# Kernel optimization log

Hardware: AMD Instinct MI355X
Metric: run time of the kernel (lower is better)

Reference implementation:

```python
import jax, jax.numpy as jnp
import numpy as np
import math

B, H, W, C = 8, 64, 64, 512
HEADS, DHEAD = 8, 64
LN_EPS = 1e-5


def layer_norm(x, g, b):
    mu = jnp.mean(x, axis=-1, keepdims=True)
    var = jnp.var(x, axis=-1, keepdims=True)
    return (x - mu) * jax.lax.rsqrt(var + LN_EPS) * g + b


def l2norm(x):
    n = jnp.sqrt(jnp.sum(x * x, axis=-1, keepdims=True))
    return x / jnp.maximum(n, 1e-12)


def dwconv3x3(x, w):
    # x: (B,C,H,W), w: (C,1,3,3) depthwise
    return jax.lax.conv_general_dilated(
        x, w, window_strides=(1, 1), padding='SAME',
        feature_group_count=x.shape[1],
        dimension_numbers=('NCHW', 'OIHW', 'NCHW'))


def setup_inputs() -> dict:
    key = jax.random.key(0)
    ks = jax.random.split(key, 16)
    s = 1.0 / math.sqrt(C)
    inp = {
        'x_in': jax.random.normal(ks[0], (B, H, W, C), jnp.float32),
        'illu_fea_trans': jax.random.normal(ks[1], (B, H, W, C), jnp.float32),
        'sem_fea_trans': jax.random.normal(ks[2], (B, H, W, C), jnp.float32),
        # SIF 1x1 convs as (C_in, C_out) matrices
        'Wk_sif': jax.random.normal(ks[3], (C, C), jnp.float32) * s,
        'Wq_sif': jax.random.normal(ks[4], (C, C), jnp.float32) * s,
        'Wv_sif': jax.random.normal(ks[5], (C, C), jnp.float32) * s,
        'ln_g': jnp.ones((C,), jnp.float32),
        'ln_b': jnp.zeros((C,), jnp.float32),
        # FG_MSA linears (in, out)
        'Wq': jax.random.normal(ks[6], (C, HEADS * DHEAD), jnp.float32) * s,
        'Wk': jax.random.normal(ks[7], (C, HEADS * DHEAD), jnp.float32) * s,
        'Wv': jax.random.normal(ks[8], (C, HEADS * DHEAD), jnp.float32) * s,
        'rescale': jnp.ones((HEADS, 1, 1), jnp.float32),
        'proj_w': jax.random.normal(ks[9], (HEADS * DHEAD, C), jnp.float32) * s,
        'proj_b': jnp.zeros((C,), jnp.float32),
        # depthwise conv pos-emb
        'dw1': jax.random.normal(ks[10], (C, 1, 3, 3), jnp.float32) * (1.0 / 3.0),
        'dw2': jax.random.normal(ks[11], (C, 1, 3, 3), jnp.float32) * (1.0 / 3.0),
    }
    return inp


def sif(illu, sem, Wk_sif, Wq_sif, Wv_sif, ln_g, ln_b):
    # illu, sem: (B, N, C); channel (C x C) cross-attention
    Kn = layer_norm(illu @ Wk_sif, ln_g, ln_b)          # (B,N,C)
    Qn = layer_norm(sem @ Wq_sif, ln_g, ln_b)           # (B,N,C)
    V = illu @ Wv_sif                                    # (B,N,C)
    Ab = jnp.einsum('bni,bnj->bij', Qn, Kn) / math.sqrt(C)  # (B,C,C)
    Ab = jax.nn.softmax(Ab, axis=-1)
    # (Ab @ V^T)^T + V ; SIF_FFN treated as identity (source not provided)
    return jnp.einsum('bij,bnj->bni', Ab, V) + V


def reference(x_in, illu_fea_trans, sem_fea_trans, Wk_sif, Wq_sif, Wv_sif,
              ln_g, ln_b, Wq, Wk, Wv, rescale, proj_w, proj_b, dw1, dw2):
    b, h, w, c = x_in.shape
    n = h * w
    x = x_in.reshape(b, n, c)
    q_inp = x @ Wq
    k_inp = x @ Wk
    v_inp = x @ Wv

    prior = sif(illu_fea_trans.reshape(b, n, c), sem_fea_trans.reshape(b, n, c),
                Wk_sif, Wq_sif, Wv_sif, ln_g, ln_b)      # (B,N,C)

    def split_heads(t):  # (b,n,h*d) -> (b,h,n,d)
        return t.reshape(b, n, HEADS, DHEAD).transpose(0, 2, 1, 3)

    q, k, v, g = map(split_heads, (q_inp, k_inp, v_inp, prior))
    v = v * g
    # transpose to (b,h,d,n), L2-normalize over n
    q = l2norm(q.transpose(0, 1, 3, 2))
    k = l2norm(k.transpose(0, 1, 3, 2))
    v = v.transpose(0, 1, 3, 2)
    attn = jnp.einsum('bhdn,bhen->bhde', k, q) * rescale  # (b,h,d,d)
    attn = jax.nn.softmax(attn, axis=-1)
    o = jnp.einsum('bhde,bhen->bhdn', attn, v)            # (b,h,d,n)
    o = o.transpose(0, 3, 1, 2).reshape(b, n, HEADS * DHEAD)
    out_c = (o @ proj_w + proj_b).reshape(b, h, w, c)

    vmap = v_inp.reshape(b, h, w, c).transpose(0, 3, 1, 2)  # NCHW
    p = dwconv3x3(vmap, dw1)
    p = jax.nn.gelu(p, approximate=False)
    p = dwconv3x3(p, dw2)
    out_p = p.transpose(0, 2, 3, 1)
    return out_c + out_p
```

## Files before the change

### kernel.cpp

```cpp
#include <hip/hip_runtime.h>

typedef unsigned short u16;
typedef unsigned int   u32;
typedef __bf16 bfx8 __attribute__((ext_vector_type(8)));
typedef float  f32x4 __attribute__((ext_vector_type(4)));

__device__ __forceinline__ float b2f(u16 v) {
    union { u32 u; float f; } c; c.u = ((u32)v) << 16; return c.f;
}
__device__ __forceinline__ u16 f2bf(float f) {
    union { float f; u32 u; } c; c.f = f;
    u32 u = c.u;
    return (u16)((u + 0x7fffu + ((u >> 16) & 1u)) >> 16);
}
__device__ __forceinline__ u16 f2bf_hw(float f) {
    __bf16 h = (__bf16)f;
    return *(u16*)&h;
}

__device__ __forceinline__ void xcd_swz(int& bx, int& by, int& bz)
{
    const int gx = gridDim.x, gy = gridDim.y, gz = gridDim.z;
    const int nwg = gx * gy * gz;
    const int flat = blockIdx.x + gx * (blockIdx.y + gy * blockIdx.z);
    int w = flat;
    if ((nwg & 7) == 0) {
        const int q = nwg >> 3;
        w = (flat & 7) * q + (flat >> 3);
    }
    by = w % gy;
    const int t = w / gy;
    bx = t % gx;
    bz = t / gx;
}

__global__ void detect_dtype(const u16* __restrict__ x, int* __restrict__ flag)
{
    const int tid = threadIdx.x;
    int cnt = 0;
    for (int i = tid; i < 2048; i += 256) {
        const u16 v = x[2 * i];
        const int e = (v >> 7) & 0xFF;
        if ((v & 0x7fff) == 0 || (e >= 96 && e <= 144)) cnt++;
    }
#pragma unroll
    for (int off = 32; off > 0; off >>= 1) cnt += __shfl_xor(cnt, off);
    __shared__ int sred[4];
    if ((tid & 63) == 0) sred[tid >> 6] = cnt;
    __syncthreads();
    if (tid == 0) {
        const int total = sred[0] + sred[1] + sred[2] + sred[3];
        flag[0] = (total < 1024) ? 1 : 0;
    }
}

__global__ void to_bf16(const void* __restrict__ in, u16* __restrict__ out,
                        int n, const int* __restrict__ flag)
{
    const int i = blockIdx.x * 256 + threadIdx.x;
    if (i < n)
        out[i] = (*flag) ? f2bf(((const float*)in)[i]) : ((const u16*)in)[i];
}

__global__ void to_bf16_v8(const void* __restrict__ in, u16* __restrict__ out,
                           int n8, const int* __restrict__ flag)
{
    const int i = blockIdx.x * 256 + threadIdx.x;
    if (i >= n8) return;
    uint4 r;
    if (*flag) {
        const float4 f0 = ((const float4*)in)[2 * i];
        const float4 f1 = ((const float4*)in)[2 * i + 1];
        u16* u = (u16*)&r;
        u[0] = f2bf_hw(f0.x); u[1] = f2bf_hw(f0.y);
        u[2] = f2bf_hw(f0.z); u[3] = f2bf_hw(f0.w);
        u[4] = f2bf_hw(f1.x); u[5] = f2bf_hw(f1.y);
        u[6] = f2bf_hw(f1.z); u[7] = f2bf_hw(f1.w);
    } else {
        r = ((const uint4*)in)[i];
    }
    ((uint4*)out)[i] = r;
}

__global__ __launch_bounds__(256, 2)
void gemm_bt(const void* __restrict__ A, const u16* __restrict__ Bt,
             void* __restrict__ C,
             int M, int N, int K, int lda, int ldb, int ldc,
             long sAb, long sAh, long sBb, long sBh, long sCb, long sCh, int nh,
             int epi_mode, const u16* __restrict__ add1, long sAddB, long sAddH,
             int ldadd, const u16* __restrict__ mul1, const u16* __restrict__ bias,
             const int* __restrict__ aF32, const int* __restrict__ cF32)
{
    __shared__ __align__(16) u16 As[128 * 40];
    __shared__ __align__(16) u16 Bs[128 * 40];
    const bool af32 = aF32 && (*aF32 != 0);
    const bool cf32 = cF32 && (*cF32 != 0);
    int bx, by, bz;
    xcd_swz(bx, by, bz);
    const int z = bz, zb = z / nh, zh = z - zb * nh;
    const long aoff = (long)zb * sAb + (long)zh * sAh;
    Bt += (long)zb * sBb + (long)zh * sBh;
    const long coff = (long)zb * sCb + (long)zh * sCh;
    const int m0 = bx * 128, n0 = by * 128;
    const int tid = threadIdx.x, lane = tid & 63, wave = tid >> 6;
    const int wm = (wave >> 1) * 64, wn = (wave & 1) * 64;
    const int q = lane >> 4, l16 = lane & 15;
    const int rowL = tid >> 2, kcol = (tid & 3) * 8;

    f32x4 acc[4][4] = {};

    for (int k0 = 0; k0 < K; k0 += 32) {
#pragma unroll
        for (int p = 0; p < 2; ++p) {
            const int r = rowL + p * 64;
            uint4 va = {0, 0, 0, 0}, vb = {0, 0, 0, 0};
            if (m0 + r < M) {
                const long ai = aoff + (long)(m0 + r) * lda + k0 + kcol;
                if (af32) {
                    const float* Af = (const float*)A + ai;
                    float4 f0 = *(const float4*)Af;
                    float4 f1 = *(const float4*)(Af + 4);
                    u16* u = (u16*)&va;
                    u[0] = f2bf_hw(f0.x); u[1] = f2bf_hw(f0.y);
                    u[2] = f2bf_hw(f0.z); u[3] = f2bf_hw(f0.w);
                    u[4] = f2bf_hw(f1.x); u[5] = f2bf_hw(f1.y);
                    u[6] = f2bf_hw(f1.z); u[7] = f2bf_hw(f1.w);
                } else {
                    va = *(const uint4*)((const u16*)A + ai);
                }
            }
            if (n0 + r < N) vb = *(const uint4*)(Bt + (long)(n0 + r) * ldb + k0 + kcol);
            *(uint4*)(&As[r * 40 + kcol]) = va;
            *(uint4*)(&Bs[r * 40 + kcol]) = vb;
        }
        __syncthreads();
        bfx8 af[4], bfr[4];
#pragma unroll
        for (int t = 0; t < 4; ++t) {
            af[t]  = *(const bfx8*)(&As[(wm + t * 16 + l16) * 40 + q * 8]);
            bfr[t] = *(const bfx8*)(&Bs[(wn + t * 16 + l16) * 40 + q * 8]);
        }
#pragma unroll
        for (int i = 0; i < 4; ++i)
#pragma unroll
            for (int j = 0; j < 4; ++j)
                acc[i][j] = __builtin_amdgcn_mfma_f32_16x16x32_bf16(af[i], bfr[j], acc[i][j], 0, 0, 0);
        __syncthreads();
    }

#pragma unroll
    for (int i = 0; i < 4; ++i) {
#pragma unroll
        for (int j = 0; j < 4; ++j) {
#pragma unroll
            for (int r = 0; r < 4; ++r) {
                const int gm = m0 + wm + i * 16 + q * 4 + r;
                const int gn = n0 + wn + j * 16 + l16;
                if (gm < M && gn < N) {
                    float v = acc[i][j][r];
                    const long cidx = coff + (long)gm * ldc + gn;
                    if (epi_mode == 2) {
                        const long aidx = (long)zb * sAddB + (long)zh * sAddH + (long)gm * ldadd + gn;
                        v = (v + b2f(add1[aidx])) * b2f(mul1[aidx]);
                    } else if (epi_mode == 3) {
                        const long aidx = (long)gm * ldadd + gn;
                        v = v + b2f(bias[gn]) + b2f(add1[aidx]);
                    }
                    if (cf32) ((float*)C)[cidx] = v;
                    else      ((u16*)C)[cidx] = f2bf(v);
                }
            }
        }
    }
}

__global__ __launch_bounds__(256, 2)
void gemm_at(const u16* __restrict__ A, const u16* __restrict__ B,
             float* __restrict__ C,
             int M, int N, int K, int lda, int ldb, int ldc,
             long sAb, long sAh, long sBb, long sBh, long sCb, long sCh, int nh)
{
    __shared__ __align__(16) u16 At[128 * 64];
    __shared__ __align__(16) u16 Bl[128 * 64];
    int bx, by, bz;
    xcd_swz(bx, by, bz);
    const int z = bz, zb = z / nh, zh = z - zb * nh;
    A += (long)zb * sAb + (long)zh * sAh;
    B += (long)zb * sBb + (long)zh * sBh;
    const long coff = (long)zb * sCb + (long)zh * sCh;
    const int i0 = bx * 128, j0 = by * 128;
    const int tid = threadIdx.x, lane = tid & 63, wave = tid >> 6;
    const int wm = (wave >> 1) * 64, wn = (wave & 1) * 64;
    const int q = lane >> 4, l16 = lane & 15;
    const int tr = tid >> 4, tc8 = (tid & 15) * 8;
    const int sw = (tc8 >> 3) & 7;

    f32x4 acc[4][4] = {};

    for (int n0 = 0; n0 < K; n0 += 64) {
#pragma unroll
        for (int p = 0; p < 4; ++p) {
            const int nn = tr + p * 16;
            uint4 va = {0, 0, 0, 0}, vb = {0, 0, 0, 0};
            if (i0 + tc8 < M) va = *(const uint4*)(A + (long)(n0 + nn) * lda + i0 + tc8);
            if (j0 + tc8 < N) vb = *(const uint4*)(B + (long)(n0 + nn) * ldb + j0 + tc8);
            const u16* ua = (const u16*)&va;
            const u16* ub = (const u16*)&vb;
#pragma unroll
            for (int e = 0; e < 8; ++e) {
                const int k = nn ^ ((e ^ sw) << 3);
                At[(tc8 + e) * 64 + k] = ua[e];
                Bl[(tc8 + e) * 64 + k] = ub[e];
            }
        }
        __syncthreads();
#pragma unroll
        for (int ks = 0; ks < 2; ++ks) {
            bfx8 af[4], bfr[4];
#pragma unroll
            for (int t = 0; t < 4; ++t) {
                const int ra = wm + t * 16 + l16;
                const int sa = ((ra & 7) ^ ((ra >> 3) & 7)) << 3;
                af[t]  = *(const bfx8*)(&At[ra * 64 + ((ks * 32 + q * 8) ^ sa)]);
                const int rb = wn + t * 16 + l16;
                const int sb = ((rb & 7) ^ ((rb >> 3) & 7)) << 3;
                bfr[t] = *(const bfx8*)(&Bl[rb * 64 + ((ks * 32 + q * 8) ^ sb)]);
            }
#pragma unroll
            for (int i = 0; i < 4; ++i)
#pragma unroll
                for (int j = 0; j < 4; ++j)
                    acc[i][j] = __builtin_amdgcn_mfma_f32_16x16x32_bf16(af[i], bfr[j], acc[i][j], 0, 0, 0);
        }
        __syncthreads();
    }

#pragma unroll
    for (int i = 0; i < 4; ++i)
#pragma unroll
        for (int j = 0; j < 4; ++j)
#pragma unroll
            for (int r = 0; r < 4; ++r) {
                const int gm = i0 + wm + i * 16 + q * 4 + r;
                const int gn = j0 + wn + j * 16 + l16;
                if (gm < M && gn < N)
                    C[coff + (long)gm * ldc + gn] = acc[i][j][r];
            }
}

__global__ void transpose_k(const void* __restrict__ in, u16* __restrict__ out,
                            const int* __restrict__ dflag)
{
    __shared__ __align__(16) u16 tile[64 * 72];
    const bool f32 = (*dflag != 0);
    const int r0 = blockIdx.x * 64, c0 = blockIdx.y * 64;
    const int tid = threadIdx.x;
    {
        const int tr = tid >> 3, tc = (tid & 7) * 8;
#pragma unroll
        for (int p = 0; p < 2; ++p) {
            const int r = tr + p * 32;
            const long base = (long)(r0 + r) * 512 + c0 + tc;
#pragma unroll
            for (int e = 0; e < 8; ++e) {
                tile[r * 72 + tc + e] = f32 ? f2bf(((const float*)in)[base + e])
                                            : ((const u16*)in)[base + e];
            }
        }
    }
    __syncthreads();
    {
        const int oc = tid >> 3, rn = (tid & 7) * 8;
#pragma unroll
        for (int p = 0; p < 2; ++p) {
            const int c = oc + p * 32;
            u16 res[8];
#pragma unroll
            for (int i = 0; i < 8; ++i) res[i] = tile[(rn + i) * 72 + c];
            *(uint4*)(out + (long)(c0 + c) * 512 + r0 + rn) = *(uint4*)res;
        }
    }
}

__global__ void ln_stats(const u16* __restrict__ in, float* __restrict__ mu,
                         float* __restrict__ rstd)
{
    const long row = blockIdx.x;
    const u16* p = in + row * 512;
    const int tid = threadIdx.x;
    const float v0 = b2f(p[tid * 2]), v1 = b2f(p[tid * 2 + 1]);
    float s = v0 + v1, sq = v0 * v0 + v1 * v1;
#pragma unroll
    for (int off = 32; off > 0; off >>= 1) {
        s  += __shfl_xor(s, off);
        sq += __shfl_xor(sq, off);
    }
    __shared__ float ls[4], lq[4];
    if ((tid & 63) == 0) { ls[tid >> 6] = s; lq[tid >> 6] = sq; }
    __syncthreads();
    if (tid == 0) {
        s = ls[0] + ls[1] + ls[2] + ls[3];
        sq = lq[0] + lq[1] + lq[2] + lq[3];
        const float m = s * (1.0f / 512.0f);
        float var = sq * (1.0f / 512.0f) - m * m;
        var = fmaxf(var, 0.0f);
        mu[row] = m;
        rstd[row] = rsqrtf(var + 1e-5f);
    }
}

__global__ void ln_apply(u16* __restrict__ x, const float* __restrict__ mu,
                         const float* __restrict__ rstd,
                         const u16* __restrict__ g, const u16* __restrict__ b)
{
    const long idx = (long)blockIdx.x * 256 + threadIdx.x;
    const long row = idx >> 6;
    const int  c8  = (int)(idx & 63) * 8;
    u16* p = x + row * 512 + c8;
    uint4 v = *(uint4*)p;
    u16* u = (u16*)&v;
    const float m_ = mu[row], rs = rstd[row];
#pragma unroll
    for (int i = 0; i < 8; ++i)
        u[i] = f2bf((b2f(u[i]) - m_) * rs * b2f(g[c8 + i]) + b2f(b[c8 + i]));
    *(uint4*)p = v;
}

__global__ void zero_f32(float* __restrict__ p, int n)
{
    const int i = blockIdx.x * 256 + threadIdx.x;
    if (i < n) p[i] = 0.0f;
}

__global__ void colssq(const u16* __restrict__ in, float* __restrict__ ssq, int rowsPerChunk)
{
    const int b = blockIdx.x, cchunk = blockIdx.y, nchunk = blockIdx.z;
    const int c = cchunk * 256 + threadIdx.x;
    const u16* p = in + (long)b * 4096 * 512 + (long)nchunk * rowsPerChunk * 512 + c;
    float acc = 0.f;
    for (int n = 0; n < rowsPerChunk; ++n) {
        const float v = b2f(p[(long)n * 512]);
        acc += v * v;
    }
    atomicAdd(&ssq[b * 512 + c], acc);
}

__global__ void softmax_ab(const float* __restrict__ Ab, u16* __restrict__ out,
                           long sstride, int nsplit)
{
    const long row = blockIdx.x;
    const float* p = Ab + row * 512;
    const int tid = threadIdx.x;
    const float scale = 0.044194173824159216f;
    float a = 0.f, b = 0.f;
    for (int s = 0; s < nsplit; ++s) {
        a += p[(long)s * sstride + tid];
        b += p[(long)s * sstride + tid + 256];
    }
    a *= scale; b *= scale;
    float m = fmaxf(a, b);
#pragma unroll
    for (int off = 32; off > 0; off >>= 1) m = fmaxf(m, __shfl_xor(m, off));
    __shared__ float red[8];
    if ((tid & 63) == 0) red[tid >> 6] = m;
    __syncthreads();
    m = fmaxf(fmaxf(red[0], red[1]), fmaxf(red[2], red[3]));
    const float e0 = __expf(a - m), e1 = __expf(b - m);
    float s = e0 + e1;
#pragma unroll
    for (int off = 32; off > 0; off >>= 1) s += __shfl_xor(s, off);
    if ((tid & 63) == 0) red[4 + (tid >> 6)] = s;
    __syncthreads();
    s = red[4] + red[5] + red[6] + red[7];
    const float inv = 1.0f / fmaxf(s, 1e-30f);
    out[row * 512 + tid]       = f2bf(e0 * inv);
    out[row * 512 + tid + 256] = f2bf(e1 * inv);
}

__global__ void softmax_g(const float* __restrict__ G, const u16* __restrict__ rescale,
                          const float* __restrict__ ssq_k, const float* __restrict__ ssq_q,
                          u16* __restrict__ out, long sstride, int nsplit)
{
    const int row = blockIdx.x * 4 + (threadIdx.x >> 6);
    const int lane = threadIdx.x & 63;
    const int zz = row >> 6, d = row & 63;
    const int b_ = zz >> 3, h = zz & 7;
    const float rk = 1.0f / fmaxf(sqrtf(fmaxf(ssq_k[b_ * 512 + h * 64 + d], 0.f)), 1e-12f);
    const float rq = 1.0f / fmaxf(sqrtf(fmaxf(ssq_q[b_ * 512 + h * 64 + lane], 0.f)), 1e-12f);
    float gv = 0.f;
    for (int s = 0; s < nsplit; ++s)
        gv += G[(long)s * sstride + (long)row * 64 + lane];
    const float v = gv * rk * rq * b2f(rescale[h]);
    float m = v;
#pragma unroll
    for (int off = 32; off > 0; off >>= 1) m = fmaxf(m, __shfl_xor(m, off));
    const float e = __expf(v - m);
    float s = e;
#pragma unroll
    for (int off = 32; off > 0; off >>= 1) s += __shfl_xor(s, off);
    out[(long)row * 64 + lane] = f2bf(e / fmaxf(s, 1e-30f));
}

__global__ void dwconv3x3(const u16* __restrict__ in, const u16* __restrict__ w,
                          u16* __restrict__ out, int do_gelu)
{
    __shared__ u16 wl[4608];
    const int tid = threadIdx.x;
    for (int i = tid; i < 4608; i += 256) wl[i] = w[i];
    __syncthreads();
    const int b = blockIdx.x >> 6, y = blockIdx.x & 63;
    const long base = (long)b * 64 * 64 * 512;
    for (int t = 0; t < 16; ++t) {
        const int idx = t * 256 + tid;
        const int cg = idx & 63, x = idx >> 6;
        float acc[8] = {};
#pragma unroll
        for (int dy = -1; dy <= 1; ++dy) {
            const int yy = y + dy;
            if (yy < 0 || yy > 63) continue;
#pragma unroll
            for (int dx = -1; dx <= 1; ++dx) {
                const int xx = x + dx;
                if (xx < 0 || xx > 63) continue;
                const uint4 v = *(const uint4*)(in + base + ((long)yy * 64 + xx) * 512 + cg * 8);
                const u16* u = (const u16*)&v;
                const int wo = (dy + 1) * 3 + (dx + 1);
#pragma unroll
                for (int i = 0; i < 8; ++i)
                    acc[i] += b2f(u[i]) * b2f(wl[(cg * 8 + i) * 9 + wo]);
            }
        }
        u16 res[8];
#pragma unroll
        for (int i = 0; i < 8; ++i) {
            float v = acc[i];
            if (do_gelu) v = 0.5f * v * (1.0f + erff(v * 0.70710678118654752f));
            res[i] = f2bf(v);
        }
        *(uint4*)(out + base + ((long)y * 64 + x) * 512 + cg * 8) = *(uint4*)res;
    }
}

extern "C" void kernel_launch(void* const* d_in, const int* in_sizes, int n_in,
                              void* d_out, int out_size, void* d_ws, size_t ws_size,
                              hipStream_t stream)
{
    const void* x     = d_in[0];
    const void* illu  = d_in[1];
    const void* sem   = d_in[2];
    const void* WkS   = d_in[3];
    const void* WqS   = d_in[4];
    const void* WvS   = d_in[5];
    const void* ln_g  = d_in[6];
    const void* ln_b  = d_in[7];
    const void* Wq    = d_in[8];
    const void* Wk    = d_in[9];
    const void* Wv    = d_in[10];
    const void* resc  = d_in[11];
    const void* projW = d_in[12];
    const void* projB = d_in[13];
    const void* dw1   = d_in[14];
    const void* dw2   = d_in[15];
    (void)in_sizes; (void)n_in; (void)out_size; (void)ws_size;

    char* ws = (char*)d_ws;
    size_t off = 0;
    auto nxt = [&](size_t bytes) -> void* {
        void* p = ws + off;
        off += (bytes + 255) & ~(size_t)255;
        return p;
    };

    u16* WqT   = (u16*)nxt(524288);
    u16* WkT   = (u16*)nxt(524288);
    u16* WvT   = (u16*)nxt(524288);
    u16* WkST  = (u16*)nxt(524288);
    u16* WqST  = (u16*)nxt(524288);
    u16* WvST  = (u16*)nxt(524288);
    u16* projT = (u16*)nxt(524288);
    u16* A = (u16*)nxt(33554432);
    u16* B = (u16*)nxt(33554432);
    u16* C = (u16*)nxt(33554432);
    float* Abf  = (float*)nxt(8388608);
    u16*   Absm = (u16*)nxt(4194304);
    float* mu   = (float*)nxt(131072);
    float* rs   = (float*)nxt(131072);
    float* ssq_q = (float*)nxt(16384);
    float* ssq_k = (float*)nxt(16384);
    float* Gf   = (float*)nxt(1048576);
    u16*   attn = (u16*)nxt(524288);
    int*   dflag = (int*)nxt(256);
    u16* ln_gc  = (u16*)nxt(1024);
    u16* ln_bc  = (u16*)nxt(1024);
    u16* projBc = (u16*)nxt(1024);
    u16* rescc  = (u16*)nxt(256);
    u16* dw1c   = (u16*)nxt(9216);
    u16* dw2c   = (u16*)nxt(9216);
    (void)Gf;

    const dim3 blk(256);

    detect_dtype<<<dim3(1), blk, 0, stream>>>((const u16*)x, dflag);
    to_bf16<<<dim3(2), blk, 0, stream>>>(ln_g,  ln_gc,  512,  dflag);
    to_bf16<<<dim3(2), blk, 0, stream>>>(ln_b,  ln_bc,  512,  dflag);
    to_bf16<<<dim3(2), blk, 0, stream>>>(projB, projBc, 512,  dflag);
    to_bf16<<<dim3(1), blk, 0, stream>>>(resc,  rescc,  8,    dflag);
    to_bf16<<<dim3(18), blk, 0, stream>>>(dw1,  dw1c,   4608, dflag);
    to_bf16<<<dim3(18), blk, 0, stream>>>(dw2,  dw2c,   4608, dflag);

    auto wT = [&](const void* w, u16* o) {
        transpose_k<<<dim3(8, 8, 1), blk, 0, stream>>>(w, o, dflag);
    };
    wT(Wq, WqT); wT(Wk, WkT); wT(Wv, WvT);
    wT(WkS, WkST); wT(WqS, WqST); wT(WvS, WvST); wT(projW, projT);

    auto gemm = [&](const void* Ap, const u16* Btp, void* Cp, int M, int N, int K,
                    int lda, int ldb, int ldc, int nz, int nh,
                    long sAb, long sAh, long sBb, long sBh, long sCb, long sCh,
                    int epi, const u16* add1, long sAddB, long sAddH, int ldadd,
                    const u16* mul1, const u16* bias,
                    const int* aF32, const int* cF32) {
        dim3 g((M + 127) / 128, (N + 127) / 128, nz);
        gemm_bt<<<g, blk, 0, stream>>>(Ap, Btp, Cp, M, N, K, lda, ldb, ldc,
            sAb, sAh, sBb, sBh, sCb, sCh, nh, epi, add1, sAddB, sAddH, ldadd,
            mul1, bias, aF32, cF32);
    };

    gemm(illu, WkST, A, 32768, 512, 512, 512, 512, 512, 1, 1, 0,0,0,0,0,0, 1,
         nullptr,0,0,0, nullptr, nullptr, dflag, nullptr);
    ln_stats<<<dim3(32768), blk, 0, stream>>>(A, mu, rs);
    ln_apply<<<dim3(8192), blk, 0, stream>>>(A, mu, rs, ln_gc, ln_bc);
    gemm(sem, WqST, B, 32768, 512, 512, 512, 512, 512, 1, 1, 0,0,0,0,0,0, 1,
         nullptr,0,0,0, nullptr, nullptr, dflag, nullptr);
    ln_stats<<<dim3(32768), blk, 0, stream>>>(B, mu, rs);
    ln_apply<<<dim3(8192), blk, 0, stream>>>(B, mu, rs, ln_gc, ln_bc);
    float* Cf = (float*)C;
    gemm_at<<<dim3(4, 4, 32), blk, 0, stream>>>(B, A, Cf, 512, 512, 1024,
        512, 512, 512, 524288, 2097152, 524288, 2097152, 2097152, 262144, 8);
    softmax_ab<<<dim3(4096), blk, 0, stream>>>(Cf, Absm, 2097152, 4);

    u16* xb = C;
    to_bf16_v8<<<dim3(8192), blk, 0, stream>>>(x, xb, 2097152, dflag);
    gemm(xb, WqT, A, 32768, 512, 512, 512, 512, 512, 1, 1, 0,0,0,0,0,0, 1,
         nullptr,0,0,0, nullptr, nullptr, nullptr, nullptr);
    zero_f32<<<dim3(16), blk, 0, stream>>>(ssq_q, 4096);
    colssq<<<dim3(8, 2, 16), blk, 0, stream>>>(A, ssq_q, 256);
    gemm(xb, WkT, B, 32768, 512, 512, 512, 512, 512, 1, 1, 0,0,0,0,0,0, 1,
         nullptr,0,0,0, nullptr, nullptr, nullptr, nullptr);
    zero_f32<<<dim3(16), blk, 0, stream>>>(ssq_k, 4096);
    colssq<<<dim3(8, 2, 16), blk, 0, stream>>>(B, ssq_k, 256);
    gemm_at<<<dim3(1, 1, 512), blk, 0, stream>>>(B, A, Abf, 64, 64, 512,
        512, 512, 64, 262144, 64, 262144, 64, 262144, 4096, 64);
    softmax_g<<<dim3(1024), blk, 0, stream>>>(Abf, rescc, ssq_k, ssq_q, attn,
        262144, 8);

    gemm(xb, WvT, A, 32768, 512, 512, 512, 512, 512, 1, 1, 0,0,0,0,0,0, 1,
         nullptr,0,0,0, nullptr, nullptr, nullptr, nullptr);
    gemm(illu, WvST, B, 32768, 512, 512, 512, 512, 512, 1, 1, 0,0,0,0,0,0, 1,
         nullptr,0,0,0, nullptr, nullptr, dflag, nullptr);
    gemm(B, Absm, C, 4096, 512, 512, 512, 512, 512, 8, 1,
         2097152, 0, 262144, 0, 2097152, 0, 2, B, 2097152, 0, 512, A, nullptr,
         nullptr, nullptr);
    gemm(C, attn, B, 4096, 64, 64, 512, 64, 512, 64, 8,
         2097152, 64, 32768, 4096, 2097152, 64, 1, nullptr,0,0,0, nullptr, nullptr,
         nullptr, nullptr);
    dwconv3x3<<<dim3(512), blk, 0, stream>>>(A, dw1c, C, 1);
    dwconv3x3<<<dim3(512), blk, 0, stream>>>(C, dw2c, A, 0);
    gemm(B, projT, d_out, 32768, 512, 512, 512, 512, 512, 1, 1, 0,0,0,0,0,0,
         3, A, 0, 0, 512, nullptr, projBc, nullptr, dflag);
}
```

Baseline: 1.040 ms.

## Add direct global-to-LDS GEMM path, pre-convert inputs to bf16, fuse layer norm

Adds a new GEMM kernel that loads A and B tiles straight into LDS with global_load_lds and an XOR-swizzled layout. It drops the fp32-input branch and padded shared tiles, so fp32 inputs (illu, sem) are now converted to bf16 in a separate pass before their GEMMs. Layer-norm stats and apply are fused into one kernel that handles one row per wave, with no shared-memory reduction. The new GEMM has no double buffering and adds extra conversion passes, and it assumes M and N are multiples of 128.

Result: faster. 937.0 us (-9.9%).

```diff
diff --git a/kernel.cpp b/kernel.cpp
--- a/kernel.cpp
+++ b/kernel.cpp
@@ -16,6 +16,13 @@
 __device__ __forceinline__ u16 f2bf_hw(float f) {
     __bf16 h = (__bf16)f;
     return *(u16*)&h;
+}
+
+__device__ __forceinline__ void gld_lds16(const u16* g, u16* l)
+{
+    __builtin_amdgcn_global_load_lds(
+        (const __attribute__((address_space(1))) void*)g,
+        (__attribute__((address_space(3))) void*)l, 16, 0, 0);
 }
 
 __device__ __forceinline__ void xcd_swz(int& bx, int& by, int& bz)
@@ -80,6 +87,88 @@
         r = ((const uint4*)in)[i];
     }
     ((uint4*)out)[i] = r;
+}
+
+__global__ __launch_bounds__(256, 2)
+void gemm_btf(const u16* __restrict__ A, const u16* __restrict__ Bt,
+              void* __restrict__ C,
+              int M, int N, int K, int lda, int ldb, int ldc,
+              long sAb, long sAh, long sBb, long sBh, long sCb, long sCh, int nh,
+              int epi_mode, const u16* __restrict__ add1, long sAddB, long sAddH,
+              int ldadd, const u16* __restrict__ mul1, const u16* __restrict__ bias,
+              const int* __restrict__ cF32)
+{
+    __shared__ __align__(16) u16 As[128 * 32];
+    __shared__ __align__(16) u16 Bs[128 * 32];
+    const bool cf32 = cF32 && (*cF32 != 0);
+    int bx, by, bz;
+    xcd_swz(bx, by, bz);
+    const int zb = bz / nh, zh = bz - zb * nh;
+    const int m0 = bx * 128, n0 = by * 128;
+    const int tid = threadIdx.x, lane = tid & 63, wave = tid >> 6;
+    const int wm = (wave >> 1) * 64, wn = (wave & 1) * 64;
+    const int q = lane >> 4, l16 = lane & 15;
+
+    const int r0 = tid >> 2, c0 = tid & 3;
+    const int cs = (c0 ^ ((r0 >> 1) & 3)) * 8;
+    const u16* pA = A + (long)zb * sAb + (long)zh * sAh;
+    const u16* pB = Bt + (long)zb * sBb + (long)zh * sBh;
+    const u16* gA0 = pA + (long)(m0 + r0) * lda + cs;
+    const u16* gA1 = pA + (long)(m0 + r0 + 64) * lda + cs;
+    const u16* gB0 = pB + (long)(n0 + r0) * ldb + cs;
+    const u16* gB1 = pB + (long)(n0 + r0 + 64) * ldb + cs;
+    u16* lA0 = &As[tid * 8];
+    u16* lA1 = &As[(256 + tid) * 8];
+    u16* lB0 = &Bs[tid * 8];
+    u16* lB1 = &Bs[(256 + tid) * 8];
+
+    const int fco = (q ^ ((l16 >> 1) & 3)) * 8;
+
+    f32x4 acc[4][4] = {};
+
+    for (int k0 = 0; k0 < K; k0 += 32) {
+        gld_lds16(gA0 + k0, lA0);
+        gld_lds16(gA1 + k0, lA1);
+        gld_lds16(gB0 + k0, lB0);
+        gld_lds16(gB1 + k0, lB1);
+        __syncthreads();
+        bfx8 af[4], bfr[4];
+#pragma unroll
+        for (int t = 0; t < 4; ++t) {
+            af[t]  = *(const bfx8*)(&As[(wm + t * 16 + l16) * 32 + fco]);
+            bfr[t] = *(const bfx8*)(&Bs[(wn + t * 16 + l16) * 32 + fco]);
+        }
+#pragma unroll
+        for (int i = 0; i < 4; ++i)
+#pragma unroll
+            for (int j = 0; j < 4; ++j)
+                acc[i][j] = __builtin_amdgcn_mfma_f32_16x16x32_bf16(af[i], bfr[j], acc[i][j], 0, 0, 0);
+        __syncthreads();
+    }
+
+    const long coff = (long)zb * sCb + (long)zh * sCh;
+#pragma unroll
+    for (int i = 0; i < 4; ++i) {
+#pragma unroll
+        for (int j = 0; j < 4; ++j) {
+#pragma unroll
+            for (int r = 0; r < 4; ++r) {
+                const int gm = m0 + wm + i * 16 + q * 4 + r;
+                const int gn = n0 + wn + j * 16 + l16;
+                float v = acc[i][j][r];
+                const long cidx = coff + (long)gm * ldc + gn;
+                if (epi_mode == 2) {
+                    const long aidx = (long)zb * sAddB + (long)zh * sAddH + (long)gm * ldadd + gn;
+                    v = (v + b2f(add1[aidx])) * b2f(mul1[aidx]);
+                } else if (epi_mode == 3) {
+                    const long aidx = (long)gm * ldadd + gn;
+                    v = v + b2f(bias[gn]) + b2f(add1[aidx]);
+                }
+                if (cf32) ((float*)C)[cidx] = v;
+                else      ((u16*)C)[cidx] = f2bf(v);
+            }
+        }
+    }
 }
 
 __global__ __launch_bounds__(256, 2)
@@ -282,47 +371,31 @@
     }
 }
 
-__global__ void ln_stats(const u16* __restrict__ in, float* __restrict__ mu,
-                         float* __restrict__ rstd)
-{
-    const long row = blockIdx.x;
-    const u16* p = in + row * 512;
-    const int tid = threadIdx.x;
-    const float v0 = b2f(p[tid * 2]), v1 = b2f(p[tid * 2 + 1]);
-    float s = v0 + v1, sq = v0 * v0 + v1 * v1;
+__global__ void ln_fused(u16* __restrict__ x, const u16* __restrict__ g,
+                         const u16* __restrict__ b)
+{
+    const long row = (long)blockIdx.x * 4 + (threadIdx.x >> 6);
+    const int lane = threadIdx.x & 63;
+    const int c8 = lane * 8;
+    u16* p = x + row * 512 + c8;
+    uint4 v = *(uint4*)p;
+    u16* u = (u16*)&v;
+    float f[8];
+    float s = 0.f, sq = 0.f;
+#pragma unroll
+    for (int i = 0; i < 8; ++i) { f[i] = b2f(u[i]); s += f[i]; sq += f[i] * f[i]; }
 #pragma unroll
     for (int off = 32; off > 0; off >>= 1) {
         s  += __shfl_xor(s, off);
         sq += __shfl_xor(sq, off);
     }
-    __shared__ float ls[4], lq[4];
-    if ((tid & 63) == 0) { ls[tid >> 6] = s; lq[tid >> 6] = sq; }
-    __syncthreads();
-    if (tid == 0) {
-        s = ls[0] + ls[1] + ls[2] + ls[3];
-        sq = lq[0] + lq[1] + lq[2] + lq[3];
-        const float m = s * (1.0f / 512.0f);
-        float var = sq * (1.0f / 512.0f) - m * m;
-        var = fmaxf(var, 0.0f);
-        mu[row] = m;
-        rstd[row] = rsqrtf(var + 1e-5f);
-    }
-}
-
-__global__ void ln_apply(u16* __restrict__ x, const float* __restrict__ mu,
-                         const float* __restrict__ rstd,
-                         const u16* __restrict__ g, const u16* __restrict__ b)
-{
-    const long idx = (long)blockIdx.x * 256 + threadIdx.x;
-    const long row = idx >> 6;
-    const int  c8  = (int)(idx & 63) * 8;
-    u16* p = x + row * 512 + c8;
-    uint4 v = *(uint4*)p;
-    u16* u = (u16*)&v;
-    const float m_ = mu[row], rs = rstd[row];
+    const float m = s * (1.0f / 512.0f);
+    float var = sq * (1.0f / 512.0f) - m * m;
+    var = fmaxf(var, 0.0f);
+    const float rs = rsqrtf(var + 1e-5f);
 #pragma unroll
     for (int i = 0; i < 8; ++i)
-        u[i] = f2bf((b2f(u[i]) - m_) * rs * b2f(g[c8 + i]) + b2f(b[c8 + i]));
+        u[i] = f2bf((f[i] - m) * rs * b2f(g[c8 + i]) + b2f(b[c8 + i]));
     *(uint4*)p = v;
 }
 
@@ -496,7 +569,7 @@
     u16* rescc  = (u16*)nxt(256);
     u16* dw1c   = (u16*)nxt(9216);
     u16* dw2c   = (u16*)nxt(9216);
-    (void)Gf;
+    (void)Gf; (void)mu; (void)rs;
 
     const dim3 blk(256);
 
@@ -514,26 +587,25 @@
     wT(Wq, WqT); wT(Wk, WkT); wT(Wv, WvT);
     wT(WkS, WkST); wT(WqS, WqST); wT(WvS, WvST); wT(projW, projT);
 
-    auto gemm = [&](const void* Ap, const u16* Btp, void* Cp, int M, int N, int K,
-                    int lda, int ldb, int ldc, int nz, int nh,
-                    long sAb, long sAh, long sBb, long sBh, long sCb, long sCh,
-                    int epi, const u16* add1, long sAddB, long sAddH, int ldadd,
-                    const u16* mul1, const u16* bias,
-                    const int* aF32, const int* cF32) {
-        dim3 g((M + 127) / 128, (N + 127) / 128, nz);
-        gemm_bt<<<g, blk, 0, stream>>>(Ap, Btp, Cp, M, N, K, lda, ldb, ldc,
+    auto gemmf = [&](const u16* Ap, const u16* Btp, void* Cp, int M, int N, int K,
+                     int lda, int ldb, int ldc, int nz, int nh,
+                     long sAb, long sAh, long sBb, long sBh, long sCb, long sCh,
+                     int epi, const u16* add1, long sAddB, long sAddH, int ldadd,
+                     const u16* mul1, const u16* bias, const int* cF32) {
+        dim3 g(M / 128, N / 128, nz);
+        gemm_btf<<<g, blk, 0, stream>>>(Ap, Btp, Cp, M, N, K, lda, ldb, ldc,
             sAb, sAh, sBb, sBh, sCb, sCh, nh, epi, add1, sAddB, sAddH, ldadd,
-            mul1, bias, aF32, cF32);
+            mul1, bias, cF32);
     };
 
-    gemm(illu, WkST, A, 32768, 512, 512, 512, 512, 512, 1, 1, 0,0,0,0,0,0, 1,
-         nullptr,0,0,0, nullptr, nullptr, dflag, nullptr);
-    ln_stats<<<dim3(32768), blk, 0, stream>>>(A, mu, rs);
-    ln_apply<<<dim3(8192), blk, 0, stream>>>(A, mu, rs, ln_gc, ln_bc);
-    gemm(sem, WqST, B, 32768, 512, 512, 512, 512, 512, 1, 1, 0,0,0,0,0,0, 1,
-         nullptr,0,0,0, nullptr, nullptr, dflag, nullptr);
-    ln_stats<<<dim3(32768), blk, 0, stream>>>(B, mu, rs);
-    ln_apply<<<dim3(8192), blk, 0, stream>>>(B, mu, rs, ln_gc, ln_bc);
+    to_bf16_v8<<<dim3(8192), blk, 0, stream>>>(illu, C, 2097152, dflag);
+    gemmf(C, WkST, A, 32768, 512, 512, 512, 512, 512, 1, 1, 0,0,0,0,0,0, 1,
+          nullptr,0,0,0, nullptr, nullptr, nullptr);
+    ln_fused<<<dim3(8192), blk, 0, stream>>>(A, ln_gc, ln_bc);
+    to_bf16_v8<<<dim3(8192), blk, 0, stream>>>(sem, C, 2097152, dflag);
+    gemmf(C, WqST, B, 32768, 512, 512, 512, 512, 512, 1, 1, 0,0,0,0,0,0, 1,
+          nullptr,0,0,0, nullptr, nullptr, nullptr);
+    ln_fused<<<dim3(8192), blk, 0, stream>>>(B, ln_gc, ln_bc);
     float* Cf = (float*)C;
     gemm_at<<<dim3(4, 4, 32), blk, 0, stream>>>(B, A, Cf, 512, 512, 1024,
         512, 512, 512, 524288, 2097152, 524288, 2097152, 2097152, 262144, 8);
@@ -541,12 +613,12 @@
 
     u16* xb = C;
     to_bf16_v8<<<dim3(8192), blk, 0, stream>>>(x, xb, 2097152, dflag);
-    gemm(xb, WqT, A, 32768, 512, 512, 512, 512, 512, 1, 1, 0,0,0,0,0,0, 1,
-         nullptr,0,0,0, nullptr, nullptr, nullptr, nullptr);
+    gemmf(xb, WqT, A, 32768, 512, 512, 512, 512, 512, 1, 1, 0,0,0,0,0,0, 1,
+          nullptr,0,0,0, nullptr, nullptr, nullptr);
     zero_f32<<<dim3(16), blk, 0, stream>>>(ssq_q, 4096);
     colssq<<<dim3(8, 2, 16), blk, 0, stream>>>(A, ssq_q, 256);
-    gemm(xb, WkT, B, 32768, 512, 512, 512, 512, 512, 1, 1, 0,0,0,0,0,0, 1,
-         nullptr,0,0,0, nullptr, nullptr, nullptr, nullptr);
+    gemmf(xb, WkT, B, 32768, 512, 512, 512, 512, 512, 1, 1, 0,0,0,0,0,0, 1,
+          nullptr,0,0,0, nullptr, nullptr, nullptr);
     zero_f32<<<dim3(16), blk, 0, stream>>>(ssq_k, 4096);
     colssq<<<dim3(8, 2, 16), blk, 0, stream>>>(B, ssq_k, 256);
     gemm_at<<<dim3(1, 1, 512), blk, 0, stream>>>(B, A, Abf, 64, 64, 512,
@@ -554,18 +626,19 @@
     softmax_g<<<dim3(1024), blk, 0, stream>>>(Abf, rescc, ssq_k, ssq_q, attn,
         262144, 8);
 
-    gemm(xb, WvT, A, 32768, 512, 512, 512, 512, 512, 1, 1, 0,0,0,0,0,0, 1,
-         nullptr,0,0,0, nullptr, nullptr, nullptr, nullptr);
-    gemm(illu, WvST, B, 32768, 512, 512, 512, 512, 512, 1, 1, 0,0,0,0,0,0, 1,
-         nullptr,0,0,0, nullptr, nullptr, dflag, nullptr);
-    gemm(B, Absm, C, 4096, 512, 512, 512, 512, 512, 8, 1,
-         2097152, 0, 262144, 0, 2097152, 0, 2, B, 2097152, 0, 512, A, nullptr,
-         nullptr, nullptr);
-    gemm(C, attn, B, 4096, 64, 64, 512, 64, 512, 64, 8,
-         2097152, 64, 32768, 4096, 2097152, 64, 1, nullptr,0,0,0, nullptr, nullptr,
-         nullptr, nullptr);
+    gemmf(xb, WvT, A, 32768, 512, 512, 512, 512, 512, 1, 1, 0,0,0,0,0,0, 1,
+          nullptr,0,0,0, nullptr, nullptr, nullptr);
+    to_bf16_v8<<<dim3(8192), blk, 0, stream>>>(illu, C, 2097152, dflag);
+    gemmf(C, WvST, B, 32768, 512, 512, 512, 512, 512, 1, 1, 0,0,0,0,0,0, 1,
+          nullptr,0,0,0, nullptr, nullptr, nullptr);
+    gemmf(B, Absm, C, 4096, 512, 512, 512, 512, 512, 8, 1,
+          2097152, 0, 262144, 0, 2097152, 0, 2, B, 2097152, 0, 512, A, nullptr,
+          nullptr);
+    gemm_bt<<<dim3(32, 1, 64), blk, 0, stream>>>(C, attn, B, 4096, 64, 64,
+        512, 64, 512, 2097152, 64, 32768, 4096, 2097152, 64, 8,
+        1, nullptr, 0, 0, 0, nullptr, nullptr, nullptr, nullptr);
     dwconv3x3<<<dim3(512), blk, 0, stream>>>(A, dw1c, C, 1);
     dwconv3x3<<<dim3(512), blk, 0, stream>>>(C, dw2c, A, 0);
-    gemm(B, projT, d_out, 32768, 512, 512, 512, 512, 512, 1, 1, 0,0,0,0,0,0,
-         3, A, 0, 0, 512, nullptr, projBc, nullptr, dflag);
-}
+    gemmf(B, projT, d_out, 32768, 512, 512, 512, 512, 512, 1, 1, 0,0,0,0,0,0,
+          3, A, 0, 0, 512, nullptr, projBc, dflag);
+}
```
